# Kernel optimization log

Measured on AMD Instinct MI355X. Metric: run time of the kernel, lower is better.

Reference implementation:

```python
import jax, jax.numpy as jnp
import numpy as np

NUM_CLASSES = 80
NUM_ANCHORS = 5
ANCHORS = np.array([[1.3221, 1.73145], [3.19275, 4.00944], [5.05587, 8.09892],
                    [9.47112, 4.84053], [11.2364, 10.0071]], dtype=np.float32)
OBJECT_SCALE = 5.0
NOOBJECT_SCALE = 1.0
COORD_SCALE = 1.0
CLASS_SCALE = 1.0
THRESH = 0.6
SEEN = 0  # module initializes self.seen = 0 -> burn-in branch (seen < 12800) active
MAX_BOXES = 50


def _iou_cxcywh(a, b):
    # a, b: (..., 4) center-x, center-y, w, h; broadcastable. Matches multi_bbox_ious(x1y1x2y2=False).
    ax1, ax2 = a[..., 0] - a[..., 2] / 2, a[..., 0] + a[..., 2] / 2
    ay1, ay2 = a[..., 1] - a[..., 3] / 2, a[..., 1] + a[..., 3] / 2
    bx1, bx2 = b[..., 0] - b[..., 2] / 2, b[..., 0] + b[..., 2] / 2
    by1, by2 = b[..., 1] - b[..., 3] / 2, b[..., 1] + b[..., 3] / 2
    iw = jnp.maximum(jnp.minimum(ax2, bx2) - jnp.maximum(ax1, bx1), 0.0)
    ih = jnp.maximum(jnp.minimum(ay2, by2) - jnp.maximum(ay1, by1), 0.0)
    inter = iw * ih
    union = a[..., 2] * a[..., 3] + b[..., 2] * b[..., 3] - inter
    return inter / jnp.maximum(union, 1e-10)


def setup_inputs() -> dict:
    key = jax.random.key(0)
    k1, k2, k3, k4, k5, k6 = jax.random.split(key, 6)
    nB, nH, nW = 64, 38, 38
    output = jax.random.normal(k1, (nB, NUM_ANCHORS * (5 + NUM_CLASSES), nH, nW), dtype=jnp.float32)
    # target rows: (class, x, y, w, h), coords normalized to (0,1); x>0 keeps all 50 boxes valid
    cls = jax.random.randint(k2, (nB, MAX_BOXES), 0, NUM_CLASSES).astype(jnp.float32)
    x = jax.random.uniform(k3, (nB, MAX_BOXES), minval=0.05, maxval=0.95)
    y = jax.random.uniform(k4, (nB, MAX_BOXES), minval=0.05, maxval=0.95)
    w = jax.random.uniform(k5, (nB, MAX_BOXES), minval=0.02, maxval=0.4)
    h = jax.random.uniform(k6, (nB, MAX_BOXES), minval=0.02, maxval=0.4)
    target = jnp.stack([cls, x, y, w, h], axis=-1).reshape(nB, MAX_BOXES * 5)
    return {"output": output, "target": target}


def _forward(output, target):
    nB, nA, nC = output.shape[0], NUM_ANCHORS, NUM_CLASSES
    nH, nW = output.shape[2], output.shape[3]
    N = nB * nA * nH * nW
    anchors = jnp.asarray(ANCHORS)
    f32 = output.dtype

    out5 = output.reshape(nB, nA, 5 + nC, nH, nW)
    txy = jax.nn.sigmoid(out5[:, :, 0:2])  # [nB,nA,2,nH,nW]
    twh = out5[:, :, 2:4]
    conf = jax.nn.sigmoid(out5[:, :, 4]).reshape(N)
    cls_logits = out5[:, :, 5:].transpose(0, 1, 3, 4, 2).reshape(N, nC)
    # coord layout matches torch: [4, nB*nA*nH*nW], rows = (sx, sy, tw, th)
    coord = jnp.concatenate([txy, twh], axis=2).transpose(2, 0, 1, 3, 4).reshape(4, N)

    # decoded pred boxes in grid units; detached like the original (convert2cpu + .detach())
    grid_x = jnp.arange(nW, dtype=f32)
    grid_y = jnp.arange(nH, dtype=f32)[:, None]
    px = txy[:, :, 0] + grid_x
    py = txy[:, :, 1] + grid_y
    pw = jnp.exp(twh[:, :, 0]) * anchors[:, 0][None, :, None, None]
    ph = jnp.exp(twh[:, :, 1]) * anchors[:, 1][None, :, None, None]
    pred_boxes = jax.lax.stop_gradient(jnp.stack([px, py, pw, ph], axis=-1))  # [nB,nA,nH,nW,4]

    # ---------------- build_targets, vectorized over (batch, gt-box) ----------------
    tbox = target.reshape(nB, MAX_BOXES, 5)  # (cls, x, y, w, h)
    # loop breaks at first x == 0 -> prefix-valid mask
    valid = jnp.cumprod((tbox[:, :, 1] > 0).astype(jnp.int32), axis=1).astype(bool)
    gx, gy = tbox[:, :, 1] * nW, tbox[:, :, 2] * nH
    gw, gh = tbox[:, :, 3] * nW, tbox[:, :, 4] * nH
    gt = jnp.stack([gx, gy, gw, gh], axis=-1)  # [nB,50,4]

    # pass 1: ignore mask -- max IoU of every pred box against all valid GTs
    pb_flat = pred_boxes.reshape(nB, nA * nH * nW, 4)
    ious = _iou_cxcywh(pb_flat[:, :, None, :], gt[:, None, :, :])  # [nB,P,50]
    cur_ious = jnp.where(valid[:, None, :], ious, 0.0).max(axis=2)
    noobj = (cur_ious <= THRESH).astype(f32).reshape(N)

    # pass 2: best anchor per GT (both boxes centered at origin -> IoU simplifies)
    aw, ah = anchors[:, 0], anchors[:, 1]
    inter_a = jnp.minimum(aw, gw[..., None]) * jnp.minimum(ah, gh[..., None])  # [nB,50,nA]
    union_a = aw * ah + (gw * gh)[..., None] - inter_a
    best_n = jnp.argmax(inter_a / jnp.maximum(union_a, 1e-10), axis=-1)  # [nB,50]

    gi = jnp.clip(gx.astype(jnp.int32), 0, nW - 1)
    gj = jnp.clip(gy.astype(jnp.int32), 0, nH - 1)
    b_idx = jnp.arange(nB)[:, None]
    pred_sel = pred_boxes[b_idx, best_n, gj, gi]  # [nB,50,4]
    iou_sel = _iou_cxcywh(gt, pred_sel)           # [nB,50]

    fidx = ((b_idx * nA + best_n) * nH + gj) * nW + gi
    fidx = jnp.where(valid, fidx, N)  # invalid boxes -> OOB index, dropped by scatter

    obj = jnp.zeros(N, f32).at[fidx].set(1.0, mode='drop')
    noobj = noobj.at[fidx].set(0.0, mode='drop')
    cm0 = 0.01 if SEEN < 12800 else 0.0
    coord_mask = jnp.full(N, cm0, f32).at[fidx].set(2.0 - tbox[:, :, 3] * tbox[:, :, 4], mode='drop')
    t0 = 0.5 if SEEN < 12800 else 0.0
    tc0 = jnp.full(N, t0, f32).at[fidx].set(gx - gi.astype(f32), mode='drop')
    tc1 = jnp.full(N, t0, f32).at[fidx].set(gy - gj.astype(f32), mode='drop')
    tc2 = jnp.zeros(N, f32).at[fidx].set(jnp.log(gw / aw[best_n]), mode='drop')
    tc3 = jnp.zeros(N, f32).at[fidx].set(jnp.log(gh / ah[best_n]), mode='drop')
    tcoord = jnp.stack([tc0, tc1, tc2, tc3], axis=0)  # [4,N]
    tconf = jnp.zeros(N, f32).at[fidx].set(iou_sel, mode='drop')  # rescore=1
    tcls = jnp.zeros(N, jnp.int32).at[fidx].set(tbox[:, :, 0].astype(jnp.int32), mode='drop')

    # ---------------- losses ----------------
    conf_mask = OBJECT_SCALE * obj + NOOBJECT_SCALE * noobj
    loss_coord = COORD_SCALE * jnp.sum(((coord - tcoord) * coord_mask) ** 2) / nB
    loss_conf = jnp.sum(((conf - tconf) * conf_mask) ** 2) / nB
    logp = jax.nn.log_softmax(cls_logits, axis=-1)
    ce = -jnp.take_along_axis(logp, tcls[:, None], axis=1)[:, 0]  # per-cell CE
    loss_cls = CLASS_SCALE * jnp.sum(obj * ce) / nB  # CE summed only over obj cells
    return loss_coord + loss_conf + loss_cls


def reference(output, target):
    return _forward(output, target)
```

## Files before the change

### kernel.cpp

```cpp
#include <hip/hip_runtime.h>
#include <math.h>

#define NB 64
#define NA 5
#define NC 80
#define NH 38
#define NW 38
#define MAXB 50
#define PLANE (NH*NW)
#define PER_B (NA*PLANE)
#define NCH (5+NC)
#define MAIN_BX ((PER_B + 255) / 256)
#define NPART (MAIN_BX * NB)

__constant__ float c_aw[5] = {1.3221f, 3.19275f, 5.05587f, 9.47112f, 11.2364f};
__constant__ float c_ah[5] = {1.73145f, 4.00944f, 8.09892f, 4.84053f, 10.0071f};

struct Entry {
    int   fidx;
    int   tcls;
    float cm, tc0, tc1, tc2, tc3, tconf;
};

__device__ inline float fexp(float x)     { return __expf(x); }
__device__ inline float flog(float x)     { return __logf(x); }
__device__ inline float fsigmoid(float x) { return __builtin_amdgcn_rcpf(1.f + __expf(-x)); }

__global__ __launch_bounds__(256)
void main_kernel(const float* __restrict__ out, const float* __restrict__ target,
                 float* __restrict__ partial) {
    const int b   = blockIdx.y;
    const int bx  = blockIdx.x;
    const int tid = threadIdx.x;

    __shared__ float4 sbox[MAXB];
    __shared__ float  sarea[MAXB];
    __shared__ Entry  sent[MAXB];
    __shared__ int    sfx[64];
    __shared__ int    snv;
    __shared__ int    sobj_cnt;
    __shared__ int    sobj_idx[MAXB];
    __shared__ short  smap[256];

    if (tid == 0) sobj_cnt = 0;
    smap[tid] = -1;

    if (tid < 64) {
        const float* tb = target + b * MAXB * 5;
        int t = tid;
        bool has = (t < MAXB);
        float cls = 0.f, x = 0.f, y = 0.f, w = 0.f, h = 0.f;
        if (has) {
            cls = tb[t * 5 + 0];
            x   = tb[t * 5 + 1];
            y   = tb[t * 5 + 2];
            w   = tb[t * 5 + 3];
            h   = tb[t * 5 + 4];
        }
        unsigned long long mask = __ballot(has && (x > 0.f));
        bool valid = has && (((~mask) & ((1ull << (t + 1)) - 1ull)) == 0ull);

        float gx = x * NW, gy = y * NH, gw = w * NW, gh = h * NH;

        int best = 0; float bestr = -1.f;
        #pragma unroll
        for (int a = 0; a < NA; a++) {
            float inter = fminf(c_aw[a], gw) * fminf(c_ah[a], gh);
            float uni   = c_aw[a] * c_ah[a] + gw * gh - inter;
            float r = inter / fmaxf(uni, 1e-10f);
            if (r > bestr) { bestr = r; best = a; }
        }
        int gi = min(max((int)gx, 0), NW - 1);
        int gj = min(max((int)gy, 0), NH - 1);
        int fidx = b * PER_B + best * PLANE + gj * NW + gi;

        float iou_sel = 0.f;
        if (valid) {
            int base = ((b * NA + best) * NCH) * PLANE + gj * NW + gi;
            float o0 = out[base];
            float o1 = out[base + PLANE];
            float o2 = out[base + 2 * PLANE];
            float o3 = out[base + 3 * PLANE];
            float px = fsigmoid(o0) + (float)gi;
            float py = fsigmoid(o1) + (float)gj;
            float pw = fexp(o2) * c_aw[best];
            float ph = fexp(o3) * c_ah[best];
            float iw = fmaxf(fminf(gx + gw*0.5f, px + pw*0.5f) - fmaxf(gx - gw*0.5f, px - pw*0.5f), 0.f);
            float ih = fmaxf(fminf(gy + gh*0.5f, py + ph*0.5f) - fmaxf(gy - gh*0.5f, py - ph*0.5f), 0.f);
            float inter = iw * ih;
            float uni = gw * gh + pw * ph - inter;
            iou_sel = inter / fmaxf(uni, 1e-10f);
        }

        sfx[t] = valid ? fidx : -1;
        bool winner = valid;
        if (valid) {
            for (int s = t + 1; s < MAXB; s++)
                if (sfx[s] == fidx) { winner = false; break; }
        }

        if (has) {
            sbox[t]  = make_float4(gx - gw*0.5f, gy - gh*0.5f, gx + gw*0.5f, gy + gh*0.5f);
            sarea[t] = gw * gh;
            Entry e;
            e.fidx  = winner ? fidx : -1;
            e.tcls  = (int)cls;
            e.cm    = 2.f - w * h;
            e.tc0   = gx - (float)gi;
            e.tc1   = gy - (float)gj;
            e.tc2   = flog(gw / c_aw[best]);
            e.tc3   = flog(gh / c_ah[best]);
            e.tconf = iou_sel;
            sent[t] = e;
        }
        if (t == 0) {
            unsigned long long nm = ~mask;
            snv = min(__ffsll((unsigned long long)nm) - 1, MAXB);
        }
    }
    __syncthreads();

    const int nlo = b * PER_B + bx * 256;
    if (tid < MAXB) {
        int f = sent[tid].fidx;
        if (f >= nlo && f < nlo + 256) {
            int slot = atomicAdd(&sobj_cnt, 1);
            sobj_idx[slot] = tid;
            smap[f - nlo] = (short)tid;
        }
    }
    __syncthreads();

    const int wid = tid >> 6, lane = tid & 63;
    const int oc = sobj_cnt;

    int   my_e = (wid < oc) ? sobj_idx[wid] : -1;
    float v1 = 0.f, v2 = -INFINITY;
    int   my_tcls = 0;
    if (my_e >= 0) {
        Entry ent = sent[my_e];
        my_tcls = ent.tcls;
        int rel  = ent.fidx - b * PER_B;
        int a    = rel / PLANE;
        int pos  = rel - a * PLANE;
        const float* cp = out + ((b * NA + a) * NCH + 5) * PLANE + pos;
        v1 = cp[lane * PLANE];
        if (lane < NC - 64) v2 = cp[(64 + lane) * PLANE];
    }

    int m = bx * 256 + tid;
    float part = 0.f;
    if (m < PER_B) {
        int a   = m / PLANE;
        int pos = m - a * PLANE;
        int j   = pos / NW;
        int i   = pos - j * NW;

        int base = ((b * NA + a) * NCH) * PLANE + pos;
        float o0 = out[base];
        float o1 = out[base + PLANE];
        float o2 = out[base + 2 * PLANE];
        float o3 = out[base + 3 * PLANE];
        float o4 = out[base + 4 * PLANE];

        float s0   = fsigmoid(o0);
        float s1   = fsigmoid(o1);
        float conf = fsigmoid(o4);
        float pw = fexp(o2) * c_aw[a];
        float ph = fexp(o3) * c_ah[a];
        float px1 = s0 + (float)i - pw * 0.5f;
        float px2 = px1 + pw;
        float py1 = s1 + (float)j - ph * 0.5f;
        float py2 = py1 + ph;
        float area_p = pw * ph;

        bool gt06 = false;
        int nv = snv;
        for (int s = 0; s < nv; s++) {
            float4 g = sbox[s];
            float iw = fmaxf(fminf(px2, g.z) - fmaxf(px1, g.x), 0.f);
            float ih = fmaxf(fminf(py2, g.w) - fmaxf(py1, g.y), 0.f);
            float inter = iw * ih;
            float uni = area_p + sarea[s] - inter;
            gt06 = gt06 || (inter > 0.6f * fmaxf(uni, 1e-10f));
        }

        float cm = 0.01f, tc0 = 0.5f, tc1 = 0.5f, tc2 = 0.f, tc3 = 0.f, tconf = 0.f;
        bool is_obj = false;
        int e = smap[tid];
        if (e >= 0) {
            is_obj = true;
            cm  = sent[e].cm;
            tc0 = sent[e].tc0;  tc1 = sent[e].tc1;
            tc2 = sent[e].tc2;  tc3 = sent[e].tc3;
            tconf = sent[e].tconf;
        }
        float conf_mask = is_obj ? 5.f : (gt06 ? 0.f : 1.f);

        float d;
        d = (s0   - tc0)   * cm;        part += d * d;
        d = (s1   - tc1)   * cm;        part += d * d;
        d = (o2   - tc2)   * cm;        part += d * d;
        d = (o3   - tc3)   * cm;        part += d * d;
        d = (conf - tconf) * conf_mask; part += d * d;
    }

    if (my_e >= 0) {
        float mx = fmaxf(v1, v2);
        for (int off = 32; off > 0; off >>= 1) mx = fmaxf(mx, __shfl_xor(mx, off));
        float s = fexp(v1 - mx) + ((lane < NC - 64) ? fexp(v2 - mx) : 0.f);
        for (int off = 32; off > 0; off >>= 1) s += __shfl_xor(s, off);
        float tv = (my_tcls < 64) ? __shfl(v1, my_tcls) : __shfl(v2, my_tcls - 64);
        if (lane == 0) part += mx + flog(s) - tv;
    }
    for (int e = 4 + wid; e < oc; e += 4) {
        Entry ent = sent[sobj_idx[e]];
        int rel  = ent.fidx - b * PER_B;
        int a    = rel / PLANE;
        int pos  = rel - a * PLANE;
        const float* cp = out + ((b * NA + a) * NCH + 5) * PLANE + pos;
        float w1 = cp[lane * PLANE];
        float w2 = (lane < NC - 64) ? cp[(64 + lane) * PLANE] : -INFINITY;
        float mx = fmaxf(w1, w2);
        for (int off = 32; off > 0; off >>= 1) mx = fmaxf(mx, __shfl_xor(mx, off));
        float s = fexp(w1 - mx) + ((lane < NC - 64) ? fexp(w2 - mx) : 0.f);
        for (int off = 32; off > 0; off >>= 1) s += __shfl_xor(s, off);
        float tv = (ent.tcls < 64) ? __shfl(w1, ent.tcls) : __shfl(w2, ent.tcls - 64);
        if (lane == 0) part += mx + flog(s) - tv;
    }

    for (int off = 32; off > 0; off >>= 1) part += __shfl_down(part, off);
    __shared__ float wsum[4];
    if (lane == 0) wsum[wid] = part;
    __syncthreads();
    if (tid == 0)
        partial[b * MAIN_BX + bx] = wsum[0] + wsum[1] + wsum[2] + wsum[3];
}

__global__ __launch_bounds__(256)
void final_kernel(const float* __restrict__ partial, float* __restrict__ loss) {
    int tid = threadIdx.x;
    float s = 0.f;
    for (int i = tid; i < NPART; i += 256) s += partial[i];
    for (int off = 32; off > 0; off >>= 1) s += __shfl_down(s, off);
    __shared__ float wsum[4];
    int wid = tid >> 6, lane = tid & 63;
    if (lane == 0) wsum[wid] = s;
    __syncthreads();
    if (tid == 0)
        loss[0] = (wsum[0] + wsum[1] + wsum[2] + wsum[3]) * (1.0f / NB);
}

extern "C" void kernel_launch(void* const* d_in, const int* in_sizes, int n_in,
                              void* d_out, int out_size, void* d_ws, size_t ws_size,
                              hipStream_t stream) {
    const float* out    = (const float*)d_in[0];
    const float* target = (const float*)d_in[1];
    float* loss    = (float*)d_out;
    float* partial = (float*)d_ws;

    dim3 grid(MAIN_BX, NB);
    main_kernel<<<grid, 256, 0, stream>>>(out, target, partial);
    final_kernel<<<1, 256, 0, stream>>>(partial, loss);
}
```

Baseline: 213.9 us.

## Process two cells per thread with fewer blocks and simplified IoU threshold test

```diff
diff --git a/kernel.cpp b/kernel.cpp
--- a/kernel.cpp
+++ b/kernel.cpp
@@ -10,7 +10,8 @@
 #define PLANE (NH*NW)
 #define PER_B (NA*PLANE)
 #define NCH (5+NC)
-#define MAIN_BX ((PER_B + 255) / 256)
+#define CPB 482
+#define MAIN_BX 15
 #define NPART (MAIN_BX * NB)
 
 __constant__ float c_aw[5] = {1.3221f, 3.19275f, 5.05587f, 9.47112f, 11.2364f};
@@ -40,10 +41,11 @@
     __shared__ int    snv;
     __shared__ int    sobj_cnt;
     __shared__ int    sobj_idx[MAXB];
-    __shared__ short  smap[256];
+    __shared__ short  smap[CPB];
 
     if (tid == 0) sobj_cnt = 0;
     smap[tid] = -1;
+    if (tid < CPB - 256) smap[256 + tid] = -1;
 
     if (tid < 64) {
         const float* tb = target + b * MAXB * 5;
@@ -101,7 +103,7 @@
 
         if (has) {
             sbox[t]  = make_float4(gx - gw*0.5f, gy - gh*0.5f, gx + gw*0.5f, gy + gh*0.5f);
-            sarea[t] = gw * gh;
+            sarea[t] = 0.6f * gw * gh;
             Entry e;
             e.fidx  = winner ? fidx : -1;
             e.tcls  = (int)cls;
@@ -120,10 +122,11 @@
     }
     __syncthreads();
 
-    const int nlo = b * PER_B + bx * 256;
+    const int cbase = bx * CPB;
+    const int nlo   = b * PER_B + cbase;
     if (tid < MAXB) {
         int f = sent[tid].fidx;
-        if (f >= nlo && f < nlo + 256) {
+        if (f >= nlo && f < nlo + CPB) {
             int slot = atomicAdd(&sobj_cnt, 1);
             sobj_idx[slot] = tid;
             smap[f - nlo] = (short)tid;
@@ -134,90 +137,132 @@
     const int wid = tid >> 6, lane = tid & 63;
     const int oc = sobj_cnt;
 
-    int   my_e = (wid < oc) ? sobj_idx[wid] : -1;
-    float v1 = 0.f, v2 = -INFINITY;
-    int   my_tcls = 0;
-    if (my_e >= 0) {
-        Entry ent = sent[my_e];
-        my_tcls = ent.tcls;
-        int rel  = ent.fidx - b * PER_B;
-        int a    = rel / PLANE;
-        int pos  = rel - a * PLANE;
+    int   eA = (wid < oc) ? sobj_idx[wid] : -1;
+    int   eB = (wid + 4 < oc) ? sobj_idx[wid + 4] : -1;
+    float vA1 = 0.f, vA2 = -INFINITY, vB1 = 0.f, vB2 = -INFINITY;
+    if (eA >= 0) {
+        int rel = sent[eA].fidx - b * PER_B;
+        int a = rel / PLANE, pos = rel - a * PLANE;
         const float* cp = out + ((b * NA + a) * NCH + 5) * PLANE + pos;
-        v1 = cp[lane * PLANE];
-        if (lane < NC - 64) v2 = cp[(64 + lane) * PLANE];
-    }
-
-    int m = bx * 256 + tid;
+        vA1 = cp[lane * PLANE];
+        if (lane < NC - 64) vA2 = cp[(64 + lane) * PLANE];
+    }
+    if (eB >= 0) {
+        int rel = sent[eB].fidx - b * PER_B;
+        int a = rel / PLANE, pos = rel - a * PLANE;
+        const float* cp = out + ((b * NA + a) * NCH + 5) * PLANE + pos;
+        vB1 = cp[lane * PLANE];
+        if (lane < NC - 64) vB2 = cp[(64 + lane) * PLANE];
+    }
+
+    int  c0 = cbase + tid;
+    int  c1 = cbase + 256 + tid;
+    bool act0 = (c0 < PER_B);
+    bool act1 = (tid < CPB - 256) && (c1 < PER_B);
+
+    int a0 = 0, i0 = 0, j0 = 0, a1 = 0, i1 = 0, j1 = 0;
+    float o0_0=0.f,o1_0=0.f,o2_0=0.f,o3_0=0.f,o4_0=0.f;
+    float o0_1=0.f,o1_1=0.f,o2_1=0.f,o3_1=0.f,o4_1=0.f;
+    if (act0) {
+        a0 = c0 / PLANE; int pos = c0 - a0 * PLANE;
+        j0 = pos / NW;   i0 = pos - j0 * NW;
+        const float* p = out + ((b * NA + a0) * NCH) * PLANE + pos;
+        o0_0 = p[0]; o1_0 = p[PLANE]; o2_0 = p[2*PLANE]; o3_0 = p[3*PLANE]; o4_0 = p[4*PLANE];
+    }
+    if (act1) {
+        a1 = c1 / PLANE; int pos = c1 - a1 * PLANE;
+        j1 = pos / NW;   i1 = pos - j1 * NW;
+        const float* p = out + ((b * NA + a1) * NCH) * PLANE + pos;
+        o0_1 = p[0]; o1_1 = p[PLANE]; o2_1 = p[2*PLANE]; o3_1 = p[3*PLANE]; o4_1 = p[4*PLANE];
+    }
+
+    float s0_0 = fsigmoid(o0_0), s1_0 = fsigmoid(o1_0), cf_0 = fsigmoid(o4_0);
+    float pw0 = fexp(o2_0) * c_aw[a0], ph0 = fexp(o3_0) * c_ah[a0];
+    float px1_0 = s0_0 + (float)i0 - pw0 * 0.5f, px2_0 = px1_0 + pw0;
+    float py1_0 = s1_0 + (float)j0 - ph0 * 0.5f, py2_0 = py1_0 + ph0;
+    float ap0 = 0.6f * pw0 * ph0;
+
+    float s0_1 = fsigmoid(o0_1), s1_1 = fsigmoid(o1_1), cf_1 = fsigmoid(o4_1);
+    float pw1 = fexp(o2_1) * c_aw[a1], ph1 = fexp(o3_1) * c_ah[a1];
+    float px1_1 = s0_1 + (float)i1 - pw1 * 0.5f, px2_1 = px1_1 + pw1;
+    float py1_1 = s1_1 + (float)j1 - ph1 * 0.5f, py2_1 = py1_1 + ph1;
+    float ap1 = 0.6f * pw1 * ph1;
+
+    bool g06_0 = false, g06_1 = false;
+    int nv = snv;
+    for (int s = 0; s < nv; s++) {
+        float4 g = sbox[s];
+        float sa = sarea[s];
+        float iw0 = fmaxf(fminf(px2_0, g.z) - fmaxf(px1_0, g.x), 0.f);
+        float ih0 = fmaxf(fminf(py2_0, g.w) - fmaxf(py1_0, g.y), 0.f);
+        g06_0 = g06_0 || (1.6f * iw0 * ih0 > ap0 + sa);
+        float iw1 = fmaxf(fminf(px2_1, g.z) - fmaxf(px1_1, g.x), 0.f);
+        float ih1 = fmaxf(fminf(py2_1, g.w) - fmaxf(py1_1, g.y), 0.f);
+        g06_1 = g06_1 || (1.6f * iw1 * ih1 > ap1 + sa);
+    }
+
     float part = 0.f;
-    if (m < PER_B) {
-        int a   = m / PLANE;
-        int pos = m - a * PLANE;
-        int j   = pos / NW;
-        int i   = pos - j * NW;
-
-        int base = ((b * NA + a) * NCH) * PLANE + pos;
-        float o0 = out[base];
-        float o1 = out[base + PLANE];
-        float o2 = out[base + 2 * PLANE];
-        float o3 = out[base + 3 * PLANE];
-        float o4 = out[base + 4 * PLANE];
-
-        float s0   = fsigmoid(o0);
-        float s1   = fsigmoid(o1);
-        float conf = fsigmoid(o4);
-        float pw = fexp(o2) * c_aw[a];
-        float ph = fexp(o3) * c_ah[a];
-        float px1 = s0 + (float)i - pw * 0.5f;
-        float px2 = px1 + pw;
-        float py1 = s1 + (float)j - ph * 0.5f;
-        float py2 = py1 + ph;
-        float area_p = pw * ph;
-
-        bool gt06 = false;
-        int nv = snv;
-        for (int s = 0; s < nv; s++) {
-            float4 g = sbox[s];
-            float iw = fmaxf(fminf(px2, g.z) - fmaxf(px1, g.x), 0.f);
-            float ih = fmaxf(fminf(py2, g.w) - fmaxf(py1, g.y), 0.f);
-            float inter = iw * ih;
-            float uni = area_p + sarea[s] - inter;
-            gt06 = gt06 || (inter > 0.6f * fmaxf(uni, 1e-10f));
-        }
-
-        float cm = 0.01f, tc0 = 0.5f, tc1 = 0.5f, tc2 = 0.f, tc3 = 0.f, tconf = 0.f;
+    if (act0) {
+        float cm = 0.01f, tc0 = 0.5f, tc1 = 0.5f, tc2 = 0.f, tc3 = 0.f, tcf = 0.f;
         bool is_obj = false;
         int e = smap[tid];
         if (e >= 0) {
             is_obj = true;
             cm  = sent[e].cm;
-            tc0 = sent[e].tc0;  tc1 = sent[e].tc1;
-            tc2 = sent[e].tc2;  tc3 = sent[e].tc3;
-            tconf = sent[e].tconf;
-        }
-        float conf_mask = is_obj ? 5.f : (gt06 ? 0.f : 1.f);
-
+            tc0 = sent[e].tc0; tc1 = sent[e].tc1;
+            tc2 = sent[e].tc2; tc3 = sent[e].tc3;
+            tcf = sent[e].tconf;
+        }
+        float cmask = is_obj ? 5.f : (g06_0 ? 0.f : 1.f);
         float d;
-        d = (s0   - tc0)   * cm;        part += d * d;
-        d = (s1   - tc1)   * cm;        part += d * d;
-        d = (o2   - tc2)   * cm;        part += d * d;
-        d = (o3   - tc3)   * cm;        part += d * d;
-        d = (conf - tconf) * conf_mask; part += d * d;
-    }
-
-    if (my_e >= 0) {
-        float mx = fmaxf(v1, v2);
+        d = (s0_0 - tc0) * cm;    part += d * d;
+        d = (s1_0 - tc1) * cm;    part += d * d;
+        d = (o2_0 - tc2) * cm;    part += d * d;
+        d = (o3_0 - tc3) * cm;    part += d * d;
+        d = (cf_0 - tcf) * cmask; part += d * d;
+    }
+    if (act1) {
+        float cm = 0.01f, tc0 = 0.5f, tc1 = 0.5f, tc2 = 0.f, tc3 = 0.f, tcf = 0.f;
+        bool is_obj = false;
+        int e = smap[256 + tid];
+        if (e >= 0) {
+            is_obj = true;
+            cm  = sent[e].cm;
+            tc0 = sent[e].tc0; tc1 = sent[e].tc1;
+            tc2 = sent[e].tc2; tc3 = sent[e].tc3;
+            tcf = sent[e].tconf;
+        }
+        float cmask = is_obj ? 5.f : (g06_1 ? 0.f : 1.f);
+        float d;
+        d = (s0_1 - tc0) * cm;    part += d * d;
+        d = (s1_1 - tc1) * cm;    part += d * d;
+        d = (o2_1 - tc2) * cm;    part += d * d;
+        d = (o3_1 - tc3) * cm;    part += d * d;
+        d = (cf_1 - tcf) * cmask; part += d * d;
+    }
+
+    if (eA >= 0) {
+        float mx = fmaxf(vA1, vA2);
         for (int off = 32; off > 0; off >>= 1) mx = fmaxf(mx, __shfl_xor(mx, off));
-        float s = fexp(v1 - mx) + ((lane < NC - 64) ? fexp(v2 - mx) : 0.f);
+        float s = fexp(vA1 - mx) + ((lane < NC - 64) ? fexp(vA2 - mx) : 0.f);
         for (int off = 32; off > 0; off >>= 1) s += __shfl_xor(s, off);
-        float tv = (my_tcls < 64) ? __shfl(v1, my_tcls) : __shfl(v2, my_tcls - 64);
+        int tc = sent[eA].tcls;
+        float tv = (tc < 64) ? __shfl(vA1, tc) : __shfl(vA2, tc - 64);
         if (lane == 0) part += mx + flog(s) - tv;
     }
-    for (int e = 4 + wid; e < oc; e += 4) {
+    if (eB >= 0) {
+        float mx = fmaxf(vB1, vB2);
+        for (int off = 32; off > 0; off >>= 1) mx = fmaxf(mx, __shfl_xor(mx, off));
+        float s = fexp(vB1 - mx) + ((lane < NC - 64) ? fexp(vB2 - mx) : 0.f);
+        for (int off = 32; off > 0; off >>= 1) s += __shfl_xor(s, off);
+        int tc = sent[eB].tcls;
+        float tv = (tc < 64) ? __shfl(vB1, tc) : __shfl(vB2, tc - 64);
+        if (lane == 0) part += mx + flog(s) - tv;
+    }
+    for (int e = 8 + wid; e < oc; e += 4) {
         Entry ent = sent[sobj_idx[e]];
-        int rel  = ent.fidx - b * PER_B;
-        int a    = rel / PLANE;
-        int pos  = rel - a * PLANE;
+        int rel = ent.fidx - b * PER_B;
+        int a = rel / PLANE, pos = rel - a * PLANE;
         const float* cp = out + ((b * NA + a) * NCH + 5) * PLANE + pos;
         float w1 = cp[lane * PLANE];
         float w2 = (lane < NC - 64) ? cp[(64 + lane) * PLANE] : -INFINITY;
```

New measurement: 215.1 us. About the same (+0.6%).
